# Performance work log

Measured on AMD Instinct MI355X. Metric: run time of the kernel, lower is better.

The kernel has to match this reference:

```python
import jax, jax.numpy as jnp
import numpy as np

D_MODEL = 1024
N_HEAD = 16


def setup_inputs() -> dict:
    key = jax.random.key(0)
    ks = jax.random.split(key, 11)
    B, S, D = 2, 2048, D_MODEL
    scale = 1.0 / np.sqrt(D)
    inp = {
        "query_tensor": jax.random.normal(ks[0], (B, S, D), jnp.float32),
        "key_tensor": jax.random.normal(ks[1], (B, S, D), jnp.float32),
        "value_tensor": jax.random.normal(ks[2], (B, S, D), jnp.float32),
        "w_q": jax.random.normal(ks[3], (D, D), jnp.float32) * scale,
        "b_q": jnp.zeros((D,), jnp.float32),
        "w_k": jax.random.normal(ks[4], (D, D), jnp.float32) * scale,
        "b_k": jnp.zeros((D,), jnp.float32),
        "w_v": jax.random.normal(ks[5], (D, D), jnp.float32) * scale,
        "b_v": jnp.zeros((D,), jnp.float32),
        "w_out": jax.random.normal(ks[6], (D, D), jnp.float32) * scale,
        "b_out": jnp.zeros((D,), jnp.float32),
    }
    return inp


def _split_heads(x, n_head):
    b, s, d = x.shape
    return x.reshape(b, s, n_head, d // n_head).transpose(0, 2, 1, 3)  # [b,h,s,dk]


def reference(query_tensor, key_tensor, value_tensor, w_q, b_q, w_k, b_k, w_v, b_v, w_out, b_out):
    # torch Linear: y = x @ W.T + b
    q = query_tensor @ w_q.T + b_q
    k = key_tensor @ w_k.T + b_k
    v = value_tensor @ w_v.T + b_v
    q = _split_heads(q, N_HEAD)
    k = _split_heads(k, N_HEAD)
    v = _split_heads(v, N_HEAD)
    d_k = k.shape[-1]
    scores = jnp.einsum("bhqd,bhkd->bhqk", q, k) / jnp.sqrt(jnp.float32(d_k))
    attn = jax.nn.softmax(scores, axis=-1)
    ctx = jnp.einsum("bhqk,bhkd->bhqd", attn, v)
    b, h, s, dk = ctx.shape
    ctx = ctx.transpose(0, 2, 1, 3).reshape(b, s, h * dk)
    return ctx @ w_out.T + b_out
```

## Files before the change

kernel.cpp:

```cpp
#include <hip/hip_runtime.h>
#include <hip/hip_bf16.h>

using ushort = unsigned short;

typedef __attribute__((ext_vector_type(8))) short bf16x8;
typedef __attribute__((ext_vector_type(4))) float f32x4;
typedef __attribute__((ext_vector_type(16))) float f32x16;
typedef __attribute__((ext_vector_type(4))) unsigned short u16x4;

#define DEVINL __device__ __forceinline__


static constexpr size_t WQ_O = 12582912;
static constexpr size_t WO_O = 15728640;
static constexpr size_t QB_O = 16777216;
static constexpr size_t KB_O = 20971520;
static constexpr size_t VT_O = 25165824;
static constexpr size_t CTX_O = 0;

DEVINL ushort f2bf(float f) {
  unsigned u = __builtin_bit_cast(unsigned, f);
  u += 0x7fffu + ((u >> 16) & 1u);
  return (ushort)(u >> 16);
}

DEVINL void gld16(const ushort* g, ushort* lds) {
  __builtin_amdgcn_global_load_lds(
      (const __attribute__((address_space(1))) void*)g,
      (__attribute__((address_space(3))) void*)lds, 16, 0, 0);
}

__global__ __launch_bounds__(256) void cvt_w(
    const float* __restrict__ wq, const float* __restrict__ wk,
    const float* __restrict__ wv, const float* __restrict__ wo,
    ushort* __restrict__ ws)
{
  int e = (blockIdx.x * 256 + threadIdx.x) * 8;
  const float* s;
  if      (e < 1048576) s = wq + e;
  else if (e < 2097152) s = wk + (e - 1048576);
  else if (e < 3145728) s = wv + (e - 2097152);
  else                  s = wo + (e - 3145728);
  float4 a = *(const float4*)s;
  float4 b = *(const float4*)(s + 4);
  union { u16x4 v; ushort u[4]; } r0, r1;
  r0.u[0] = f2bf(a.x); r0.u[1] = f2bf(a.y); r0.u[2] = f2bf(a.z); r0.u[3] = f2bf(a.w);
  r1.u[0] = f2bf(b.x); r1.u[1] = f2bf(b.y); r1.u[2] = f2bf(b.z); r1.u[3] = f2bf(b.w);
  *(u16x4*)(ws + WQ_O + e) = r0.v;
  *(u16x4*)(ws + WQ_O + e + 4) = r1.v;
}

template<bool CVTA>
DEVINL void gemm_core(const void* __restrict__ Av, const ushort* __restrict__ Bw,
                      const float* __restrict__ bias, void* __restrict__ Cout,
                      float scale, int omode, int row0, int col0)
{
  constexpr int K = 1024;
  __shared__ ushort As[128 * 64];
  __shared__ ushort Bs[128 * 64];
  const int t = threadIdx.x;
  const int l = t & 63;
  const int w = t >> 6;
  const int wr = w >> 1, wc = w & 1;

  const int srow = t >> 3;
  const int scol8 = (t & 7) * 8;
  const int swz_half = ((((t & 7) * 16) ^ ((srow & 7) << 4)) >> 1);

  const ushort* Ap16 = (const ushort*)Av + (size_t)(row0 + srow) * K + scol8;
  const float*  Ap32 = (const float*)Av + (size_t)(row0 + srow) * K + scol8;
  const ushort* Bp = Bw + (size_t)(col0 + srow) * K + scol8;

  bf16x8 areg[4], breg[4];
  float4 a32[4][2];
  auto loadstage = [&](int k0) {
#pragma unroll
    for (int i = 0; i < 4; ++i) {
      if constexpr (CVTA) {
        a32[i][0] = *(const float4*)(Ap32 + (size_t)(i * 32) * K + k0);
        a32[i][1] = *(const float4*)(Ap32 + (size_t)(i * 32) * K + k0 + 4);
      } else {
        areg[i] = *(const bf16x8*)(Ap16 + (size_t)(i * 32) * K + k0);
      }
      breg[i] = *(const bf16x8*)(Bp + (size_t)(i * 32) * K + k0);
    }
  };

  f32x4 acc[4][4];
#pragma unroll
  for (int i = 0; i < 4; ++i)
#pragma unroll
    for (int j = 0; j < 4; ++j) acc[i][j] = (f32x4){0.f, 0.f, 0.f, 0.f};

  loadstage(0);
#pragma unroll 1
  for (int kt = 0; kt < K / 64; ++kt) {
    __syncthreads();
#pragma unroll
    for (int i = 0; i < 4; ++i) {
      if constexpr (CVTA) {
        union { bf16x8 v; unsigned u[4]; } pk;
        asm("v_cvt_pk_bf16_f32 %0, %1, %2" : "=v"(pk.u[0]) : "v"(a32[i][0].x), "v"(a32[i][0].y));
        asm("v_cvt_pk_bf16_f32 %0, %1, %2" : "=v"(pk.u[1]) : "v"(a32[i][0].z), "v"(a32[i][0].w));
        asm("v_cvt_pk_bf16_f32 %0, %1, %2" : "=v"(pk.u[2]) : "v"(a32[i][1].x), "v"(a32[i][1].y));
        asm("v_cvt_pk_bf16_f32 %0, %1, %2" : "=v"(pk.u[3]) : "v"(a32[i][1].z), "v"(a32[i][1].w));
        *(bf16x8*)&As[(srow + i * 32) * 64 + swz_half] = pk.v;
      } else {
        *(bf16x8*)&As[(srow + i * 32) * 64 + swz_half] = areg[i];
      }
      *(bf16x8*)&Bs[(srow + i * 32) * 64 + swz_half] = breg[i];
    }
    if (kt + 1 < K / 64) loadstage((kt + 1) * 64);
    __syncthreads();
#pragma unroll
    for (int ks = 0; ks < 2; ++ks) {
      bf16x8 af[4], bfr[4];
#pragma unroll
      for (int mi = 0; mi < 4; ++mi) {
        int r = wr * 64 + mi * 16 + (l & 15);
        int cb = ((ks << 6) | ((l >> 4) << 4)) ^ ((r & 7) << 4);
        af[mi] = *(const bf16x8*)&As[r * 64 + (cb >> 1)];
      }
#pragma unroll
      for (int nj = 0; nj < 4; ++nj) {
        int r = wc * 64 + nj * 16 + (l & 15);
        int cb = ((ks << 6) | ((l >> 4) << 4)) ^ ((r & 7) << 4);
        bfr[nj] = *(const bf16x8*)&Bs[r * 64 + (cb >> 1)];
      }
#pragma unroll
      for (int mi = 0; mi < 4; ++mi)
#pragma unroll
        for (int nj = 0; nj < 4; ++nj)
          acc[mi][nj] = __builtin_amdgcn_mfma_f32_16x16x32_bf16(af[mi], bfr[nj], acc[mi][nj], 0, 0, 0);
    }
  }

  const int cl = l & 15;
#pragma unroll
  for (int mi = 0; mi < 4; ++mi) {
#pragma unroll
    for (int nj = 0; nj < 4; ++nj) {
      int n = col0 + wc * 64 + nj * 16 + cl;
      float bv = bias[n];
      int mbase = row0 + wr * 64 + mi * 16 + (l >> 4) * 4;
      if (omode == 1) {
        float* Of = (float*)Cout;
#pragma unroll
        for (int ri = 0; ri < 4; ++ri)
          Of[(size_t)(mbase + ri) * 1024 + n] = (acc[mi][nj][ri] + bv) * scale;
      } else if (omode == 0) {
        ushort* Ob = (ushort*)Cout;
        int h = n >> 6, d = n & 63;
#pragma unroll
        for (int ri = 0; ri < 4; ++ri) {
          int m = mbase + ri;
          int b = m >> 11, s = m & 2047;
          Ob[(size_t)((b * 16 + h) * 2048 + s) * 64 + d] = f2bf((acc[mi][nj][ri] + bv) * scale);
        }
      } else {
        ushort* Ob = (ushort*)Cout;
        int h = n >> 6, d = n & 63;
        int b = mbase >> 11, s = mbase & 2047;
        union { u16x4 v; ushort u[4]; } pk;
#pragma unroll
        for (int ri = 0; ri < 4; ++ri) pk.u[ri] = f2bf((acc[mi][nj][ri] + bv) * scale);
        *(u16x4*)&Ob[(size_t)((b * 16 + h) * 64 + d) * 2048 + s] = pk.v;
      }
    }
  }
}

__global__ __launch_bounds__(256, 2) void gemm_qkv(
    const float* __restrict__ xq, const float* __restrict__ xk, const float* __restrict__ xv,
    const ushort* __restrict__ ws_c, ushort* __restrict__ ws_m,
    const float* __restrict__ bq, const float* __restrict__ bk, const float* __restrict__ bv)
{
  int lin = blockIdx.z * 256 + blockIdx.y * 8 + blockIdx.x;
  int swz = (lin & 7) * 96 + (lin >> 3);
  int z = swz >> 8, rem = swz & 255;
  int by = rem >> 3, bx = rem & 7;
  const float* A = (z == 0) ? xq : ((z == 1) ? xk : xv);
  const ushort* W = ws_c + WQ_O + (size_t)z * 1048576;
  const float* bias = (z == 0) ? bq : ((z == 1) ? bk : bv);
  ushort* dst = ws_m + QB_O + (size_t)z * 4194304;
  float scale = (z == 0) ? (0.125f * 1.4426950408889634f) : 1.0f;
  int omode = (z == 2) ? 2 : 0;
  gemm_core<true>(A, W, bias, dst, scale, omode, by * 128, bx * 128);
}

__global__ __launch_bounds__(256, 2) void gemm_out(
    const ushort* __restrict__ ctx, const ushort* __restrict__ wo,
    const float* __restrict__ bo, float* __restrict__ out)
{
  int lin = blockIdx.y * 8 + blockIdx.x;
  int swz = (lin & 7) * 32 + (lin >> 3);
  int by = swz >> 3, bx = swz & 7;
  gemm_core<false>(ctx, wo, bo, out, 1.0f, 1, by * 128, bx * 128);
}

__global__ __launch_bounds__(512, 4) void attn8(
    const ushort* __restrict__ Qb, const ushort* __restrict__ Kb,
    const ushort* __restrict__ Vtb, ushort* __restrict__ Ctx)
{
  __shared__ ushort smem[32768];

  const int t = threadIdx.x, l = t & 63, w = t >> 6;
  const int wq4 = w & 3, half = w >> 2;
  const int hi2 = l >> 5, q = l & 31;
  const int bh = blockIdx.y, qt = blockIdx.x;
  const int kvb = half * 1024;
  const ushort* Qp = Qb + ((size_t)bh * 2048 + qt * 128 + wq4 * 32) * 64;
  const ushort* Kp = Kb + (size_t)bh * 2048 * 64;
  const ushort* Vp = Vtb + (size_t)bh * 64 * 2048;

  ushort* Ksh = smem + half * 8192;
  ushort* Vsh = smem + 16384 + half * 8192;

  bf16x8 qf[4];
#pragma unroll
  for (int ks = 0; ks < 4; ++ks)
    qf[ks] = *(const bf16x8*)(Qp + q * 64 + ks * 16 + hi2 * 8);

  auto stageKV = [&](int pp, int kv0) {
#pragma unroll
    for (int i = 0; i < 2; ++i) {
      int R = (i * 4 + wq4) * 8 + (l >> 3);
      int g = l & 7;
      int sR = (R & ~12) | ((R & 4) << 1) | ((R & 8) >> 1);
      gld16(Kp + (size_t)(kv0 + sR) * 64 + (g ^ (R & 7)) * 8,
            Ksh + pp * 4096 + (i * 4 + wq4) * 512);
      gld16(Vp + (size_t)R * 2048 + kv0 + (g ^ (R & 7)) * 8,
            Vsh + pp * 4096 + (i * 4 + wq4) * 512);
    }
  };

  f32x16 acc0, acc1;
#pragma unroll
  for (int i = 0; i < 16; ++i) { acc0[i] = 0.f; acc1[i] = 0.f; }
  float lrun = 0.f;

  const int rsw = (q & 7) << 4;

  stageKV(0, kvb);
  __syncthreads();

#pragma unroll 1
  for (int kt = 0; kt < 16; ++kt) {
    const int p = kt & 1;
    if (kt + 1 < 16) stageKV(p ^ 1, kvb + (kt + 1) * 64);
    const ushort* Kl = Ksh + p * 4096;
    const ushort* Vl = Vsh + p * 4096;

#pragma unroll
    for (int c = 0; c < 2; ++c) {
      f32x16 sc;
#pragma unroll
      for (int i = 0; i < 16; ++i) sc[i] = 0.f;
      const int r = c * 32 + q;
      __builtin_amdgcn_s_setprio(1);
#pragma unroll
      for (int ks = 0; ks < 4; ++ks) {
        bf16x8 kf = *(const bf16x8*)&Kl[r * 64 + (((ks * 32 + hi2 * 16) ^ rsw) >> 1)];
        sc = __builtin_amdgcn_mfma_f32_32x32x16_bf16(kf, qf[ks], sc, 0, 0, 0);
      }
      __builtin_amdgcn_s_setprio(0);

      float s0 = 0.f, s1 = 0.f, s2 = 0.f, s3 = 0.f;
#pragma unroll
      for (int i = 0; i < 4; ++i) {
        float e0 = exp2f(sc[i]);      sc[i] = e0;      s0 += e0;
        float e1 = exp2f(sc[4 + i]);  sc[4 + i] = e1;  s1 += e1;
        float e2 = exp2f(sc[8 + i]);  sc[8 + i] = e2;  s2 += e2;
        float e3 = exp2f(sc[12 + i]); sc[12 + i] = e3; s3 += e3;
      }
      lrun += (s0 + s1) + (s2 + s3);

      union PU { bf16x8 v; unsigned u[4]; } pA, pB;
#pragma unroll
      for (int i = 0; i < 4; ++i) {
        asm("v_cvt_pk_bf16_f32 %0, %1, %2" : "=v"(pA.u[i]) : "v"(sc[2 * i]), "v"(sc[2 * i + 1]));
        asm("v_cvt_pk_bf16_f32 %0, %1, %2" : "=v"(pB.u[i]) : "v"(sc[8 + 2 * i]), "v"(sc[9 + 2 * i]));
      }

      __builtin_amdgcn_s_setprio(1);
#pragma unroll
      for (int db = 0; db < 2; ++db) {
        const int d = db * 32 + q;
        bf16x8 va = *(const bf16x8*)&Vl[d * 64 + (((c * 64 + hi2 * 16) ^ rsw) >> 1)];
        bf16x8 vb = *(const bf16x8*)&Vl[d * 64 + (((c * 64 + 32 + hi2 * 16) ^ rsw) >> 1)];
        if (db == 0) {
          acc0 = __builtin_amdgcn_mfma_f32_32x32x16_bf16(va, pA.v, acc0, 0, 0, 0);
          acc0 = __builtin_amdgcn_mfma_f32_32x32x16_bf16(vb, pB.v, acc0, 0, 0, 0);
        } else {
          acc1 = __builtin_amdgcn_mfma_f32_32x32x16_bf16(va, pA.v, acc1, 0, 0, 0);
          acc1 = __builtin_amdgcn_mfma_f32_32x32x16_bf16(vb, pB.v, acc1, 0, 0, 0);
        }
      }
      __builtin_amdgcn_s_setprio(0);
    }
    __syncthreads();
  }

  float lsum = lrun + __shfl_xor(lrun, 32);
  float* red = (float*)smem;
  if (half == 1) {
    float* base = red + (wq4 * 32 + q) * 68;
#pragma unroll
    for (int db = 0; db < 2; ++db) {
#pragma unroll
      for (int g = 0; g < 4; ++g) {
        float4 v;
        if (db == 0) v = (float4){acc0[g * 4], acc0[g * 4 + 1], acc0[g * 4 + 2], acc0[g * 4 + 3]};
        else         v = (float4){acc1[g * 4], acc1[g * 4 + 1], acc1[g * 4 + 2], acc1[g * 4 + 3]};
        *(float4*)(base + db * 32 + g * 8 + hi2 * 4) = v;
      }
    }
    if (l < 32) red[8704 + wq4 * 32 + q] = lsum;
  }
  __syncthreads();
  if (half == 0) {
    const float* base = red + (wq4 * 32 + q) * 68;
    float inv = 1.0f / (lsum + red[8704 + wq4 * 32 + q]);
    const int b = bh >> 4, h = bh & 15;
    const int sg = qt * 128 + wq4 * 32 + q;
    ushort* dst = Ctx + ((size_t)b * 2048 + sg) * 1024 + h * 64;
#pragma unroll
    for (int db = 0; db < 2; ++db) {
#pragma unroll
      for (int g = 0; g < 4; ++g) {
        float4 pv = *(const float4*)(base + db * 32 + g * 8 + hi2 * 4);
        union { u16x4 v; ushort u[4]; } pk;
#pragma unroll
        for (int ri = 0; ri < 4; ++ri) {
          float a = (db == 0) ? acc0[g * 4 + ri] : acc1[g * 4 + ri];
          float p = (ri == 0) ? pv.x : (ri == 1) ? pv.y : (ri == 2) ? pv.z : pv.w;
          pk.u[ri] = f2bf((a + p) * inv);
        }
        *(u16x4*)(dst + db * 32 + g * 8 + hi2 * 4) = pk.v;
      }
    }
  }
}

extern "C" void kernel_launch(void* const* d_in, const int* in_sizes, int n_in,
                              void* d_out, int out_size, void* d_ws, size_t ws_size,
                              hipStream_t stream) {
  const float* xq = (const float*)d_in[0];
  const float* xk = (const float*)d_in[1];
  const float* xv = (const float*)d_in[2];
  const float* wq = (const float*)d_in[3];
  const float* bq = (const float*)d_in[4];
  const float* wk = (const float*)d_in[5];
  const float* bk = (const float*)d_in[6];
  const float* wv = (const float*)d_in[7];
  const float* bv = (const float*)d_in[8];
  const float* wo = (const float*)d_in[9];
  const float* bo = (const float*)d_in[10];
  ushort* ws = (ushort*)d_ws;

  cvt_w<<<2048, 256, 0, stream>>>(wq, wk, wv, wo, ws);
  gemm_qkv<<<dim3(8, 32, 3), 256, 0, stream>>>(xq, xk, xv, ws, ws, bq, bk, bv);
  attn8<<<dim3(16, 32), 512, 0, stream>>>(ws + QB_O, ws + KB_O, ws + VT_O, ws + CTX_O);
  gemm_out<<<dim3(8, 32), 256, 0, stream>>>(ws + CTX_O, ws + WO_O, bo, (float*)d_out);
}
```

Baseline: 128.6 us.

## Compute both QK score tiles before prefetching next KV tile, coalesce ctx stores

Moves both 32-row QK^T MFMA chains ahead of the next KV tile prefetch, so score computation starts before the global-to-LDS loads are issued. Replaces exp2f with the raw hardware exp2 builtin. Rewrites the epilogue to combine the two halves' partial outputs in LDS, then has all threads write row-contiguous bf16 context rows for coalesced global stores. This adds extra barriers and keeps two score accumulators live, raising register pressure.

```diff
diff --git a/kernel.cpp b/kernel.cpp
--- a/kernel.cpp
+++ b/kernel.cpp
@@ -237,6 +237,9 @@
   f32x16 acc0, acc1;
 #pragma unroll
   for (int i = 0; i < 16; ++i) { acc0[i] = 0.f; acc1[i] = 0.f; }
+  f32x16 Zv;
+#pragma unroll
+  for (int i = 0; i < 16; ++i) Zv[i] = 0.f;
   float lrun = 0.f;
 
   const int rsw = (q & 7) << 4;
@@ -247,31 +250,42 @@
 #pragma unroll 1
   for (int kt = 0; kt < 16; ++kt) {
     const int p = kt & 1;
-    if (kt + 1 < 16) stageKV(p ^ 1, kvb + (kt + 1) * 64);
     const ushort* Kl = Ksh + p * 4096;
     const ushort* Vl = Vsh + p * 4096;
 
+    f32x16 scA, scB;
+    __builtin_amdgcn_s_setprio(1);
+    {
+      bf16x8 kf = *(const bf16x8*)&Kl[q * 64 + (((hi2 * 16)) ^ rsw) / 2];
+      scA = __builtin_amdgcn_mfma_f32_32x32x16_bf16(kf, qf[0], Zv, 0, 0, 0);
+#pragma unroll
+      for (int ks = 1; ks < 4; ++ks) {
+        bf16x8 k2 = *(const bf16x8*)&Kl[q * 64 + (((ks * 32 + hi2 * 16) ^ rsw) >> 1)];
+        scA = __builtin_amdgcn_mfma_f32_32x32x16_bf16(k2, qf[ks], scA, 0, 0, 0);
+      }
+      const int r1 = (32 + q) * 64;
+      bf16x8 kg = *(const bf16x8*)&Kl[r1 + (((hi2 * 16)) ^ rsw) / 2];
+      scB = __builtin_amdgcn_mfma_f32_32x32x16_bf16(kg, qf[0], Zv, 0, 0, 0);
+#pragma unroll
+      for (int ks = 1; ks < 4; ++ks) {
+        bf16x8 k2 = *(const bf16x8*)&Kl[r1 + (((ks * 32 + hi2 * 16) ^ rsw) >> 1)];
+        scB = __builtin_amdgcn_mfma_f32_32x32x16_bf16(k2, qf[ks], scB, 0, 0, 0);
+      }
+    }
+    __builtin_amdgcn_s_setprio(0);
+
+    if (kt + 1 < 16) stageKV(p ^ 1, kvb + (kt + 1) * 64);
+
 #pragma unroll
     for (int c = 0; c < 2; ++c) {
-      f32x16 sc;
-#pragma unroll
-      for (int i = 0; i < 16; ++i) sc[i] = 0.f;
-      const int r = c * 32 + q;
-      __builtin_amdgcn_s_setprio(1);
-#pragma unroll
-      for (int ks = 0; ks < 4; ++ks) {
-        bf16x8 kf = *(const bf16x8*)&Kl[r * 64 + (((ks * 32 + hi2 * 16) ^ rsw) >> 1)];
-        sc = __builtin_amdgcn_mfma_f32_32x32x16_bf16(kf, qf[ks], sc, 0, 0, 0);
-      }
-      __builtin_amdgcn_s_setprio(0);
-
+      f32x16& sc = (c == 0) ? scA : scB;
       float s0 = 0.f, s1 = 0.f, s2 = 0.f, s3 = 0.f;
 #pragma unroll
       for (int i = 0; i < 4; ++i) {
-        float e0 = exp2f(sc[i]);      sc[i] = e0;      s0 += e0;
-        float e1 = exp2f(sc[4 + i]);  sc[4 + i] = e1;  s1 += e1;
-        float e2 = exp2f(sc[8 + i]);  sc[8 + i] = e2;  s2 += e2;
-        float e3 = exp2f(sc[12 + i]); sc[12 + i] = e3; s3 += e3;
+        float e0 = __builtin_amdgcn_exp2f(sc[i]);      sc[i] = e0;      s0 += e0;
+        float e1 = __builtin_amdgcn_exp2f(sc[4 + i]);  sc[4 + i] = e1;  s1 += e1;
+        float e2 = __builtin_amdgcn_exp2f(sc[8 + i]);  sc[8 + i] = e2;  s2 += e2;
+        float e3 = __builtin_amdgcn_exp2f(sc[12 + i]); sc[12 + i] = e3; s3 += e3;
       }
       lrun += (s0 + s1) + (s2 + s3);
 
@@ -302,11 +316,17 @@
   }
 
   float lsum = lrun + __shfl_xor(lrun, 32);
-  float* red = (float*)smem;
+  float* Lf = (float*)smem;
+
+  if (l < 32) Lf[half * 128 + wq4 * 32 + q] = lsum;
+  __syncthreads();
+  const float inv = 1.0f / (Lf[wq4 * 32 + q] + Lf[128 + wq4 * 32 + q]);
+  __syncthreads();
+
   if (half == 1) {
-    float* base = red + (wq4 * 32 + q) * 68;
-#pragma unroll
-    for (int db = 0; db < 2; ++db) {
+    float* base = Lf + (wq4 * 32 + q) * 64;
+#pragma unroll
+    for (int db = 0; db < 2; ++db)
 #pragma unroll
       for (int g = 0; g < 4; ++g) {
         float4 v;
@@ -314,30 +334,41 @@
         else         v = (float4){acc1[g * 4], acc1[g * 4 + 1], acc1[g * 4 + 2], acc1[g * 4 + 3]};
         *(float4*)(base + db * 32 + g * 8 + hi2 * 4) = v;
       }
-    }
-    if (l < 32) red[8704 + wq4 * 32 + q] = lsum;
-  }
-  __syncthreads();
+  }
+  __syncthreads();
+
   if (half == 0) {
-    const float* base = red + (wq4 * 32 + q) * 68;
-    float inv = 1.0f / (lsum + red[8704 + wq4 * 32 + q]);
+    float* base = Lf + (wq4 * 32 + q) * 64;
+#pragma unroll
+    for (int db = 0; db < 2; ++db)
+#pragma unroll
+      for (int g = 0; g < 4; ++g) {
+        float* p = base + db * 32 + g * 8 + hi2 * 4;
+        float4 pv = *(float4*)p;
+        float4 o;
+        if (db == 0) o = (float4){(acc0[g * 4] + pv.x) * inv, (acc0[g * 4 + 1] + pv.y) * inv,
+                                  (acc0[g * 4 + 2] + pv.z) * inv, (acc0[g * 4 + 3] + pv.w) * inv};
+        else         o = (float4){(acc1[g * 4] + pv.x) * inv, (acc1[g * 4 + 1] + pv.y) * inv,
+                                  (acc1[g * 4 + 2] + pv.z) * inv, (acc1[g * 4 + 3] + pv.w) * inv};
+        *(float4*)p = o;
+      }
+  }
+  __syncthreads();
+
+  {
     const int b = bh >> 4, h = bh & 15;
-    const int sg = qt * 128 + wq4 * 32 + q;
-    ushort* dst = Ctx + ((size_t)b * 2048 + sg) * 1024 + h * 64;
-#pragma unroll
-    for (int db = 0; db < 2; ++db) {
-#pragma unroll
-      for (int g = 0; g < 4; ++g) {
-        float4 pv = *(const float4*)(base + db * 32 + g * 8 + hi2 * 4);
-        union { u16x4 v; ushort u[4]; } pk;
-#pragma unroll
-        for (int ri = 0; ri < 4; ++ri) {
-          float a = (db == 0) ? acc0[g * 4 + ri] : acc1[g * 4 + ri];
-          float p = (ri == 0) ? pv.x : (ri == 1) ? pv.y : (ri == 2) ? pv.z : pv.w;
-          pk.u[ri] = f2bf((a + p) * inv);
-        }
-        *(u16x4*)(dst + db * 32 + g * 8 + hi2 * 4) = pk.v;
-      }
+    const int d0 = (l & 7) * 8;
+#pragma unroll
+    for (int rr = 0; rr < 2; ++rr) {
+      int row = w * 16 + rr * 8 + (l >> 3);
+      float4 f0 = *(const float4*)(Lf + row * 64 + d0);
+      float4 f1 = *(const float4*)(Lf + row * 64 + d0 + 4);
+      union { u16x4 v; ushort u[4]; } o0, o1;
+      o0.u[0] = f2bf(f0.x); o0.u[1] = f2bf(f0.y); o0.u[2] = f2bf(f0.z); o0.u[3] = f2bf(f0.w);
+      o1.u[0] = f2bf(f1.x); o1.u[1] = f2bf(f1.y); o1.u[2] = f2bf(f1.z); o1.u[3] = f2bf(f1.w);
+      ushort* dst = Ctx + ((size_t)b * 2048 + qt * 128 + row) * 1024 + h * 64 + d0;
+      *(u16x4*)dst = o0.v;
+      *(u16x4*)(dst + 4) = o1.v;
     }
   }
 }
```

Measured after the change: 108.8 us. 1.18x faster.
